# Kernel optimization log

Measured on AMD Instinct MI355X. Metric: run time of the kernel, lower is better.

Reference implementation:

```python
import jax, jax.numpy as jnp
import numpy as np

NUM_HEADS = 4

def setup_inputs() -> dict:
    key = jax.random.key(0)
    ks = jax.random.split(key, 9)
    total_nodes, d, hidden, B = 262144, 256, 256, 8192
    node_embeddings = jax.random.normal(ks[0], (total_nodes, d), dtype=jnp.float32)
    segment_ids = jnp.sort(jax.random.randint(ks[1], (total_nodes,), 0, B, dtype=jnp.int32))
    # learnable params (MultiheadAttention packed qkv, out_proj, query, output_proj)
    s = 0.05
    query = jax.random.normal(ks[2], (1, d), dtype=jnp.float32)
    in_proj_w = jax.random.normal(ks[3], (3 * d, d), dtype=jnp.float32) * s
    in_proj_b = jax.random.normal(ks[4], (3 * d,), dtype=jnp.float32) * s
    out_proj_w = jax.random.normal(ks[5], (d, d), dtype=jnp.float32) * s
    out_proj_b = jax.random.normal(ks[6], (d,), dtype=jnp.float32) * s
    output_proj_w = jax.random.normal(ks[7], (hidden, d), dtype=jnp.float32) * s
    output_proj_b = jax.random.normal(ks[8], (hidden,), dtype=jnp.float32) * s
    return {
        "node_embeddings": node_embeddings,
        "query": query,
        "in_proj_w": in_proj_w,
        "in_proj_b": in_proj_b,
        "out_proj_w": out_proj_w,
        "out_proj_b": out_proj_b,
        "output_proj_w": output_proj_w,
        "output_proj_b": output_proj_b,
        "segment_ids": segment_ids,
        "batch_size": B,
    }


def reference(node_embeddings, query, in_proj_w, in_proj_b, out_proj_w, out_proj_b,
              output_proj_w, output_proj_b, segment_ids, batch_size):
    # Ragged single-query cross-attention pooling (eval mode: dropout off).
    N, d = node_embeddings.shape
    H = NUM_HEADS
    dh = d // H
    Wq, Wk, Wv = in_proj_w[:d], in_proj_w[d:2 * d], in_proj_w[2 * d:]
    bq, bk, bv = in_proj_b[:d], in_proj_b[d:2 * d], in_proj_b[2 * d:]
    # query is shared across all graphs; torch MHA scales q by 1/sqrt(dh)
    q = ((query @ Wq.T + bq) / jnp.sqrt(jnp.asarray(dh, node_embeddings.dtype))).reshape(H, dh)
    k = (node_embeddings @ Wk.T + bk).reshape(N, H, dh)
    v = (node_embeddings @ Wv.T + bv).reshape(N, H, dh)
    scores = jnp.einsum('nhd,hd->nh', k, q)  # [N, H]
    # segment-wise stable softmax over ragged node groups
    m = jax.ops.segment_max(scores, segment_ids, num_segments=batch_size)  # [B, H]
    m = jnp.where(jnp.isfinite(m), m, 0.0)
    e = jnp.exp(scores - m[segment_ids])  # [N, H]
    denom = jax.ops.segment_sum(e, segment_ids, num_segments=batch_size)  # [B, H]
    numer = jax.ops.segment_sum(e[:, :, None] * v, segment_ids, num_segments=batch_size)  # [B, H, dh]
    attn = jnp.where(denom[:, :, None] > 0, numer / jnp.maximum(denom[:, :, None], 1e-30), 0.0)
    pooled = attn.reshape(batch_size, d) @ out_proj_w.T + out_proj_b  # MHA out_proj
    out = pooled @ output_proj_w.T + output_proj_b  # [B, hidden]
    # empty graphs -> zeros (matches torch branch), not just bias
    counts = jax.ops.segment_sum(jnp.ones((N,), out.dtype), segment_ids, num_segments=batch_size)
    return jnp.where(counts[:, None] > 0, out, 0.0)
```

## Files before the change

### kernel.cpp

```cpp
#include <hip/hip_runtime.h>
#include <hip/hip_bf16.h>
#include <stdint.h>

typedef __attribute__((ext_vector_type(8))) short short8;
typedef __attribute__((ext_vector_type(4))) float f32x4;

#define DEV static __device__ __forceinline__

DEV float half_red_bcast(float x) {
  int t;
  t = __builtin_amdgcn_update_dpp(0, __float_as_int(x), 0x111, 0xf, 0xf, true); x += __int_as_float(t);
  t = __builtin_amdgcn_update_dpp(0, __float_as_int(x), 0x112, 0xf, 0xf, true); x += __int_as_float(t);
  t = __builtin_amdgcn_update_dpp(0, __float_as_int(x), 0x114, 0xf, 0xf, true); x += __int_as_float(t);
  t = __builtin_amdgcn_update_dpp(0, __float_as_int(x), 0x118, 0xf, 0xf, true); x += __int_as_float(t);
  t = __builtin_amdgcn_update_dpp(0, __float_as_int(x), 0x142, 0xa, 0xf, true); x += __int_as_float(t);
  return __int_as_float(__builtin_amdgcn_ds_swizzle(__float_as_int(x), 0x3E0));
}

DEV void gload16(const void* g, void* lds) {
  __builtin_amdgcn_global_load_lds(
      (const __attribute__((address_space(1))) void*)g,
      (__attribute__((address_space(3))) void*)lds, 16, 0, 0);
}

__global__ __launch_bounds__(256) void k_prep(
    const float* __restrict__ query, const float* __restrict__ in_w,
    const float* __restrict__ in_b, const float* __restrict__ Wo,
    const float* __restrict__ bo, const float* __restrict__ Wu,
    const float* __restrict__ bu, const int* __restrict__ seg,
    float* __restrict__ wq_ws, float* __restrict__ ch_ws,
    float* __restrict__ btot, __hip_bfloat16* __restrict__ mtt,
    int* __restrict__ starts, int N, int B)
{
  __shared__ float sh[256];
  int t = threadIdx.x, bid = blockIdx.x;
  if (bid < 4) {
    float acc = in_b[t];
    for (int c = 0; c < 256; ++c) acc += query[c] * in_w[t * 256 + c];
    sh[t] = acc * 0.125f;
    __syncthreads();
    int h = bid;
    float a = 0.f;
    for (int j = 0; j < 64; ++j) a += sh[64 * h + j] * in_w[(256 + 64 * h + j) * 256 + t];
    wq_ws[h * 256 + t] = a;
    if (t == 0) {
      float c = 0.f;
      for (int j = 0; j < 64; ++j) c += sh[64 * h + j] * in_b[256 + 64 * h + j];
      ch_ws[h] = c;
    }
  } else if (bid < 260) {
    int u = bid - 4;
    float wc = 0.f;
    for (int o = 0; o < 256; ++o) wc += Wu[u * 256 + o] * Wo[o * 256 + t];
    sh[t] = wc;
    __syncthreads();
    #pragma unroll
    for (int h = 0; h < 4; ++h) {
      float a = 0.f;
      for (int r = 0; r < 64; ++r) a += sh[64 * h + r] * in_w[(512 + 64 * h + r) * 256 + t];
      mtt[(size_t)u * 1024 + h * 256 + t] = __float2bfloat16(a);
    }
  } else if (bid == 260) {
    const float* bv = in_b + 512;
    float wob = 0.f;
    for (int c = 0; c < 256; ++c) wob += Wo[t * 256 + c] * bv[c];
    sh[t] = bo[t] + wob;
    __syncthreads();
    float a = bu[t];
    for (int o = 0; o < 256; ++o) a += Wu[t * 256 + o] * sh[o];
    btot[t] = a;
  } else {
    int idx = (bid - 261) * 256 + t;
    if (idx < N) {
      int s = seg[idx];
      int prev = (idx == 0) ? -1 : seg[idx - 1];
      for (int x = prev + 1; x <= s; ++x) starts[x] = idx;
      if (idx == N - 1) for (int x = s + 1; x <= B; ++x) starts[x] = N;
    }
  }
}

__global__ __launch_bounds__(256, 4) void k_segattn(
    const float* __restrict__ emb, const int* __restrict__ starts,
    const float* __restrict__ wq_ws, const float* __restrict__ ch_ws,
    float* __restrict__ mask, __hip_bfloat16* __restrict__ T, int B)
{
  int lane = threadIdx.x & 63;
  int g = lane >> 5, i = lane & 31, i8 = i * 8;
  int b = blockIdx.x * 4 + (threadIdx.x >> 6);
  if (b >= B) return;
  int start = starts[b], end = starts[b + 1];
  __hip_bfloat16* Tb = T + (size_t)b * 1024;

  if (start >= end) {
    if (lane == 0) mask[b] = 0.f;
    if (lane < 32) {
      uint4 z = {0u, 0u, 0u, 0u};
      *(uint4*)(Tb + 0 * 256 + lane * 8) = z;
      *(uint4*)(Tb + 1 * 256 + lane * 8) = z;
      *(uint4*)(Tb + 2 * 256 + lane * 8) = z;
      *(uint4*)(Tb + 3 * 256 + lane * 8) = z;
    }
    return;
  }
  if (lane == 0) mask[b] = 1.f;

  float4 wa0 = *(const float4*)(wq_ws + 0 * 256 + i8), wb0 = *(const float4*)(wq_ws + 0 * 256 + i8 + 4);
  float4 wa1 = *(const float4*)(wq_ws + 1 * 256 + i8), wb1 = *(const float4*)(wq_ws + 1 * 256 + i8 + 4);
  float4 wa2 = *(const float4*)(wq_ws + 2 * 256 + i8), wb2 = *(const float4*)(wq_ws + 2 * 256 + i8 + 4);
  float4 wa3 = *(const float4*)(wq_ws + 3 * 256 + i8), wb3 = *(const float4*)(wq_ws + 3 * 256 + i8 + 4);
  float ch0 = ch_ws[0], ch1 = ch_ws[1], ch2 = ch_ws[2], ch3 = ch_ws[3];

  float m0 = -1e30f, m1 = -1e30f, m2 = -1e30f, m3 = -1e30f;
  float d0 = 0.f, d1 = 0.f, d2 = 0.f, d3 = 0.f;
  float4 Sa0 = {0,0,0,0}, Sb0 = {0,0,0,0}, Sa1 = {0,0,0,0}, Sb1 = {0,0,0,0};
  float4 Sa2 = {0,0,0,0}, Sb2 = {0,0,0,0}, Sa3 = {0,0,0,0}, Sb3 = {0,0,0,0};

  int r0 = start + g; if (r0 > end - 1) r0 = end - 1;
  const float* cp = emb + (size_t)r0 * 256 + i8;
  float4 c0 = *(const float4*)cp, c1 = *(const float4*)(cp + 4);

  for (int p = start; p < end; p += 2) {
    int rn = p + 2 + g; if (rn > end - 1) rn = end - 1;
    const float* np = emb + (size_t)rn * 256 + i8;
    float4 n0 = *(const float4*)np, n1 = *(const float4*)(np + 4);

    float p0 = c0.x*wa0.x + c0.y*wa0.y + c0.z*wa0.z + c0.w*wa0.w
             + c1.x*wb0.x + c1.y*wb0.y + c1.z*wb0.z + c1.w*wb0.w;
    float p1 = c0.x*wa1.x + c0.y*wa1.y + c0.z*wa1.z + c0.w*wa1.w
             + c1.x*wb1.x + c1.y*wb1.y + c1.z*wb1.z + c1.w*wb1.w;
    float p2 = c0.x*wa2.x + c0.y*wa2.y + c0.z*wa2.z + c0.w*wa2.w
             + c1.x*wb2.x + c1.y*wb2.y + c1.z*wb2.z + c1.w*wb2.w;
    float p3 = c0.x*wa3.x + c0.y*wa3.y + c0.z*wa3.z + c0.w*wa3.w
             + c1.x*wb3.x + c1.y*wb3.y + c1.z*wb3.z + c1.w*wb3.w;

    float s0 = half_red_bcast(p0) + ch0;
    float s1 = half_red_bcast(p1) + ch1;
    float s2 = half_red_bcast(p2) + ch2;
    float s3 = half_red_bcast(p3) + ch3;

    bool valid = (p + g) < end;
    if (!valid) { s0 = -1e30f; s1 = -1e30f; s2 = -1e30f; s3 = -1e30f; }

#define HEAD(s, m, d, SA, SB)                                               \
    { if (s > m) {                                                          \
        float rs = __expf(m - s);                                           \
        d *= rs;                                                            \
        SA.x *= rs; SA.y *= rs; SA.z *= rs; SA.w *= rs;                     \
        SB.x *= rs; SB.y *= rs; SB.z *= rs; SB.w *= rs;                     \
        m = s; }                                                            \
      float e = __expf(s - m);                                              \
      d += e;                                                               \
      SA.x += e * c0.x; SA.y += e * c0.y; SA.z += e * c0.z; SA.w += e * c0.w;\
      SB.x += e * c1.x; SB.y += e * c1.y; SB.z += e * c1.z; SB.w += e * c1.w; }
    HEAD(s0, m0, d0, Sa0, Sb0)
    HEAD(s1, m1, d1, Sa1, Sb1)
    HEAD(s2, m2, d2, Sa2, Sb2)
    HEAD(s3, m3, d3, Sa3, Sb3)
#undef HEAD
    c0 = n0; c1 = n1;
  }

#define FIN(mh, dh, SA, SB, h)                                              \
  { float om = __shfl_xor(mh, 32), od = __shfl_xor(dh, 32);                 \
    float mst = fmaxf(mh, om);                                              \
    float a0 = __expf(mh - mst), a1 = __expf(om - mst);                     \
    float sc = a0 / (dh * a0 + od * a1);                                    \
    float t0 = SA.x*sc, t1 = SA.y*sc, t2 = SA.z*sc, t3 = SA.w*sc;           \
    float t4 = SB.x*sc, t5 = SB.y*sc, t6 = SB.z*sc, t7 = SB.w*sc;           \
    t0 += __shfl_xor(t0, 32); t1 += __shfl_xor(t1, 32);                     \
    t2 += __shfl_xor(t2, 32); t3 += __shfl_xor(t3, 32);                     \
    t4 += __shfl_xor(t4, 32); t5 += __shfl_xor(t5, 32);                     \
    t6 += __shfl_xor(t6, 32); t7 += __shfl_xor(t7, 32);                     \
    if (g == 0) {                                                           \
      union { __hip_bfloat16 v[8]; uint4 u; } pk;                           \
      pk.v[0] = __float2bfloat16(t0); pk.v[1] = __float2bfloat16(t1);       \
      pk.v[2] = __float2bfloat16(t2); pk.v[3] = __float2bfloat16(t3);       \
      pk.v[4] = __float2bfloat16(t4); pk.v[5] = __float2bfloat16(t5);       \
      pk.v[6] = __float2bfloat16(t6); pk.v[7] = __float2bfloat16(t7);       \
      *(uint4*)(Tb + h * 256 + i8) = pk.u; } }
  FIN(m0, d0, Sa0, Sb0, 0)
  FIN(m1, d1, Sa1, Sb1, 1)
  FIN(m2, d2, Sa2, Sb2, 2)
  FIN(m3, d3, Sa3, Sb3, 3)
#undef FIN
}

__global__ __launch_bounds__(256) void k_out(
    const __hip_bfloat16* __restrict__ T, const __hip_bfloat16* __restrict__ mtt,
    const float* __restrict__ btot, const float* __restrict__ mask,
    float* __restrict__ out)
{
  __shared__ __align__(16) char smem[16384];
  char* As = smem;
  char* Bs = smem + 8192;
  int t = threadIdx.x;
  int l = t & 63, w = t >> 6;
  int wr = w >> 1, wc = w & 1;
  int tileM = blockIdx.y * 64, tileN = blockIdx.x * 64;

  const char* Tb = (const char*)T;
  const char* Mb = (const char*)mtt;
  int chunk = (l & 7) ^ ((l >> 3) & 7);
  f32x4 acc[2][2] = {};

  for (int kk = 0; kk < 1024; kk += 64) {
    #pragma unroll
    for (int i = 0; i < 2; ++i) {
      int row = (w * 2 + i) * 8 + (l >> 3);
      gload16(Tb + (size_t)(tileM + row) * 2048 + kk * 2 + chunk * 16,
              As + (w * 2 + i) * 1024);
      gload16(Mb + (size_t)(tileN + row) * 2048 + kk * 2 + chunk * 16,
              Bs + (w * 2 + i) * 1024);
    }
    __syncthreads();
    #pragma unroll
    for (int ks = 0; ks < 64; ks += 32) {
      short8 a[2], bf[2];
      int kbyte = (ks + (l >> 4) * 8) * 2;
      #pragma unroll
      for (int i = 0; i < 2; ++i) {
        int row = wr * 32 + i * 16 + (l & 15);
        a[i] = *(const short8*)(As + row * 128 + (kbyte ^ ((row & 7) << 4)));
        int crow = wc * 32 + i * 16 + (l & 15);
        bf[i] = *(const short8*)(Bs + crow * 128 + (kbyte ^ ((crow & 7) << 4)));
      }
      #pragma unroll
      for (int i = 0; i < 2; ++i)
        #pragma unroll
        for (int j = 0; j < 2; ++j)
          acc[i][j] = __builtin_amdgcn_mfma_f32_16x16x32_bf16(a[i], bf[j], acc[i][j], 0, 0, 0);
    }
    __syncthreads();
  }

  int cl = l & 15, rq = l >> 4;
  #pragma unroll
  for (int i = 0; i < 2; ++i)
    #pragma unroll
    for (int j = 0; j < 2; ++j) {
      int cg = tileN + wc * 32 + j * 16 + cl;
      float bt = btot[cg];
      #pragma unroll
      for (int r = 0; r < 4; ++r) {
        int rg = tileM + wr * 32 + i * 16 + rq * 4 + r;
        out[(size_t)rg * 256 + cg] = mask[rg] * (acc[i][j][r] + bt);
      }
    }
}

extern "C" void kernel_launch(void* const* d_in, const int* in_sizes, int n_in,
                              void* d_out, int out_size, void* d_ws, size_t ws_size,
                              hipStream_t stream) {
  const float* emb   = (const float*)d_in[0];
  const float* query = (const float*)d_in[1];
  const float* in_w  = (const float*)d_in[2];
  const float* in_b  = (const float*)d_in[3];
  const float* out_w = (const float*)d_in[4];
  const float* out_b = (const float*)d_in[5];
  const float* up_w  = (const float*)d_in[6];
  const float* up_b  = (const float*)d_in[7];
  const int*   seg   = (const int*)d_in[8];

  int N = in_sizes[0] / 256;
  int B = out_size / 256;

  char* wsb = (char*)d_ws;
  float* wq_ws  = (float*)(wsb + 0);
  float* ch_ws  = (float*)(wsb + 4096);
  float* btot   = (float*)(wsb + 8192);
  int*   starts = (int*)(wsb + 12288);
  float* maskp  = (float*)(wsb + 45312);
  __hip_bfloat16* mtt = (__hip_bfloat16*)(wsb + 78336);
  __hip_bfloat16* Tp  = (__hip_bfloat16*)(wsb + 602624);

  int nb_bounds = (N + 255) / 256;
  k_prep<<<dim3(261 + nb_bounds), dim3(256), 0, stream>>>(
      query, in_w, in_b, out_w, out_b, up_w, up_b, seg,
      wq_ws, ch_ws, btot, mtt, starts, N, B);
  k_segattn<<<dim3((B + 3) / 4), dim3(256), 0, stream>>>(
      emb, starts, wq_ws, ch_ws, maskp, Tp, B);
  k_out<<<dim3(4, B / 64), dim3(256), 0, stream>>>(Tp, mtt, btot, maskp, (float*)d_out);
}
```

Baseline: 90.17 us.

## Double-buffer LDS in output GEMM and split mtt prep across more blocks

The output GEMM kernel now uses two LDS buffers, issuing the global-to-LDS loads for the next K step before computing on the current one, so memory latency can overlap MFMA work. The prep kernel spreads the mtt weight-fusion computation over four times as many blocks, one per head, so that stage has more parallelism. The trade-off is doubled LDS per block, which may lower occupancy, and recomputing the Wu·Wo row product four times per row. There is also a possible hazard: the next stage's async LDS loads are issued with only one barrier per iteration and no explicit wait on the loads.

```diff
diff --git a/kernel.cpp b/kernel.cpp
--- a/kernel.cpp
+++ b/kernel.cpp
@@ -48,19 +48,16 @@
       for (int j = 0; j < 64; ++j) c += sh[64 * h + j] * in_b[256 + 64 * h + j];
       ch_ws[h] = c;
     }
-  } else if (bid < 260) {
-    int u = bid - 4;
+  } else if (bid < 1028) {
+    int u = (bid - 4) >> 2, h = (bid - 4) & 3;
     float wc = 0.f;
     for (int o = 0; o < 256; ++o) wc += Wu[u * 256 + o] * Wo[o * 256 + t];
     sh[t] = wc;
     __syncthreads();
-    #pragma unroll
-    for (int h = 0; h < 4; ++h) {
-      float a = 0.f;
-      for (int r = 0; r < 64; ++r) a += sh[64 * h + r] * in_w[(512 + 64 * h + r) * 256 + t];
-      mtt[(size_t)u * 1024 + h * 256 + t] = __float2bfloat16(a);
-    }
-  } else if (bid == 260) {
+    float a = 0.f;
+    for (int r = 0; r < 64; ++r) a += sh[64 * h + r] * in_w[(512 + 64 * h + r) * 256 + t];
+    mtt[(size_t)u * 1024 + h * 256 + t] = __float2bfloat16(a);
+  } else if (bid == 1028) {
     const float* bv = in_b + 512;
     float wob = 0.f;
     for (int c = 0; c < 256; ++c) wob += Wo[t * 256 + c] * bv[c];
@@ -70,7 +67,7 @@
     for (int o = 0; o < 256; ++o) a += Wu[t * 256 + o] * sh[o];
     btot[t] = a;
   } else {
-    int idx = (bid - 261) * 256 + t;
+    int idx = (bid - 1029) * 256 + t;
     if (idx < N) {
       int s = seg[idx];
       int prev = (idx == 0) ? -1 : seg[idx - 1];
@@ -191,9 +188,7 @@
     const float* __restrict__ btot, const float* __restrict__ mask,
     float* __restrict__ out)
 {
-  __shared__ __align__(16) char smem[16384];
-  char* As = smem;
-  char* Bs = smem + 8192;
+  __shared__ __align__(16) char smem[32768];
   int t = threadIdx.x;
   int l = t & 63, w = t >> 6;
   int wr = w >> 1, wc = w & 1;
@@ -202,18 +197,35 @@
   const char* Tb = (const char*)T;
   const char* Mb = (const char*)mtt;
   int chunk = (l & 7) ^ ((l >> 3) & 7);
+
+  const char* aSrc[2]; const char* bSrc[2]; int ldsOff[2];
+  #pragma unroll
+  for (int i = 0; i < 2; ++i) {
+    int row = (w * 2 + i) * 8 + (l >> 3);
+    aSrc[i] = Tb + (size_t)(tileM + row) * 2048 + chunk * 16;
+    bSrc[i] = Mb + (size_t)(tileN + row) * 2048 + chunk * 16;
+    ldsOff[i] = (w * 2 + i) * 1024;
+  }
+
   f32x4 acc[2][2] = {};
 
-  for (int kk = 0; kk < 1024; kk += 64) {
-    #pragma unroll
-    for (int i = 0; i < 2; ++i) {
-      int row = (w * 2 + i) * 8 + (l >> 3);
-      gload16(Tb + (size_t)(tileM + row) * 2048 + kk * 2 + chunk * 16,
-              As + (w * 2 + i) * 1024);
-      gload16(Mb + (size_t)(tileN + row) * 2048 + kk * 2 + chunk * 16,
-              Bs + (w * 2 + i) * 1024);
-    }
-    __syncthreads();
+#define STAGE(step, base)                                                   \
+  { int kb = (step) * 128;                                                  \
+    _Pragma("unroll")                                                       \
+    for (int i = 0; i < 2; ++i) {                                           \
+      gload16(aSrc[i] + kb, smem + (base) + ldsOff[i]);                     \
+      gload16(bSrc[i] + kb, smem + (base) + 8192 + ldsOff[i]);              \
+    } }
+
+  STAGE(0, 0);
+  __syncthreads();
+
+  int dbuf = 0;
+  for (int step = 0; step < 16; ++step) {
+    int base = dbuf << 14;
+    if (step + 1 < 16) STAGE(step + 1, base ^ 16384);
+    const char* As = smem + base;
+    const char* Bs = smem + base + 8192;
     #pragma unroll
     for (int ks = 0; ks < 64; ks += 32) {
       short8 a[2], bf[2];
@@ -232,7 +244,9 @@
           acc[i][j] = __builtin_amdgcn_mfma_f32_16x16x32_bf16(a[i], bf[j], acc[i][j], 0, 0, 0);
     }
     __syncthreads();
-  }
+    dbuf ^= 1;
+  }
+#undef STAGE
 
   int cl = l & 15, rq = l >> 4;
   #pragma unroll
@@ -275,7 +289,7 @@
   __hip_bfloat16* Tp  = (__hip_bfloat16*)(wsb + 602624);
 
   int nb_bounds = (N + 255) / 256;
-  k_prep<<<dim3(261 + nb_bounds), dim3(256), 0, stream>>>(
+  k_prep<<<dim3(1029 + nb_bounds), dim3(256), 0, stream>>>(
       query, in_w, in_b, out_w, out_b, up_w, up_b, seg,
       wq_ws, ch_ws, btot, mtt, starts, N, B);
   k_segattn<<<dim3((B + 3) / 4), dim3(256), 0, stream>>>(
```

Result: slower. 94.45 us (+4.7%).

## Move weight-folding blocks into attention kernel and use exp2 with prescaled scores

Applied to the files above, without the earlier changes.

The output-side weight folding (mtt and btot) moves out of the prep kernel and into extra blocks appended to the attention kernel's grid. That work now runs alongside the memory-bound segment attention instead of serializing ahead of it. The query/key fold is prescaled by log2(e), so the softmax can use exp2 directly and skip the multiply inside __expf. In exchange, the extra blocks take CU slots while attention runs, and the attention kernel gains shared memory and more arguments.

```diff
diff --git a/kernel.cpp b/kernel.cpp
--- a/kernel.cpp
+++ b/kernel.cpp
@@ -23,13 +23,12 @@
       (__attribute__((address_space(3))) void*)lds, 16, 0, 0);
 }
 
+#define LOG2E 1.44269504088896340736f
+
 __global__ __launch_bounds__(256) void k_prep(
     const float* __restrict__ query, const float* __restrict__ in_w,
-    const float* __restrict__ in_b, const float* __restrict__ Wo,
-    const float* __restrict__ bo, const float* __restrict__ Wu,
-    const float* __restrict__ bu, const int* __restrict__ seg,
+    const float* __restrict__ in_b, const int* __restrict__ seg,
     float* __restrict__ wq_ws, float* __restrict__ ch_ws,
-    float* __restrict__ btot, __hip_bfloat16* __restrict__ mtt,
     int* __restrict__ starts, int N, int B)
 {
   __shared__ float sh[256];
@@ -42,35 +41,14 @@
     int h = bid;
     float a = 0.f;
     for (int j = 0; j < 64; ++j) a += sh[64 * h + j] * in_w[(256 + 64 * h + j) * 256 + t];
-    wq_ws[h * 256 + t] = a;
+    wq_ws[h * 256 + t] = a * LOG2E;
     if (t == 0) {
       float c = 0.f;
       for (int j = 0; j < 64; ++j) c += sh[64 * h + j] * in_b[256 + 64 * h + j];
-      ch_ws[h] = c;
-    }
-  } else if (bid < 260) {
-    int u = bid - 4;
-    float wc = 0.f;
-    for (int o = 0; o < 256; ++o) wc += Wu[u * 256 + o] * Wo[o * 256 + t];
-    sh[t] = wc;
-    __syncthreads();
-    #pragma unroll
-    for (int h = 0; h < 4; ++h) {
-      float a = 0.f;
-      for (int r = 0; r < 64; ++r) a += sh[64 * h + r] * in_w[(512 + 64 * h + r) * 256 + t];
-      mtt[(size_t)u * 1024 + h * 256 + t] = __float2bfloat16(a);
-    }
-  } else if (bid == 260) {
-    const float* bv = in_b + 512;
-    float wob = 0.f;
-    for (int c = 0; c < 256; ++c) wob += Wo[t * 256 + c] * bv[c];
-    sh[t] = bo[t] + wob;
-    __syncthreads();
-    float a = bu[t];
-    for (int o = 0; o < 256; ++o) a += Wu[t * 256 + o] * sh[o];
-    btot[t] = a;
+      ch_ws[h] = c * LOG2E;
+    }
   } else {
-    int idx = (bid - 261) * 256 + t;
+    int idx = (bid - 4) * 256 + t;
     if (idx < N) {
       int s = seg[idx];
       int prev = (idx == 0) ? -1 : seg[idx - 1];
@@ -83,11 +61,45 @@
 __global__ __launch_bounds__(256, 4) void k_segattn(
     const float* __restrict__ emb, const int* __restrict__ starts,
     const float* __restrict__ wq_ws, const float* __restrict__ ch_ws,
-    float* __restrict__ mask, __hip_bfloat16* __restrict__ T, int B)
+    float* __restrict__ mask, __hip_bfloat16* __restrict__ T, int B, int nB,
+    const float* __restrict__ in_w, const float* __restrict__ in_b,
+    const float* __restrict__ Wo, const float* __restrict__ bo,
+    const float* __restrict__ Wu, const float* __restrict__ bu,
+    __hip_bfloat16* __restrict__ mtt, float* __restrict__ btot)
 {
-  int lane = threadIdx.x & 63;
+  __shared__ float sh[256];
+  int t = threadIdx.x;
+
+  if (blockIdx.x >= (unsigned)nB) {
+    int bid = blockIdx.x - nB;
+    if (bid < 256) {
+      int u = bid;
+      float wc = 0.f;
+      for (int o = 0; o < 256; ++o) wc += Wu[u * 256 + o] * Wo[o * 256 + t];
+      sh[t] = wc;
+      __syncthreads();
+      #pragma unroll
+      for (int h = 0; h < 4; ++h) {
+        float a = 0.f;
+        for (int r = 0; r < 64; ++r) a += sh[64 * h + r] * in_w[(512 + 64 * h + r) * 256 + t];
+        mtt[(size_t)u * 1024 + h * 256 + t] = __float2bfloat16(a);
+      }
+    } else {
+      const float* bv = in_b + 512;
+      float wob = 0.f;
+      for (int c = 0; c < 256; ++c) wob += Wo[t * 256 + c] * bv[c];
+      sh[t] = bo[t] + wob;
+      __syncthreads();
+      float a = bu[t];
+      for (int o = 0; o < 256; ++o) a += Wu[t * 256 + o] * sh[o];
+      btot[t] = a;
+    }
+    return;
+  }
+
+  int lane = t & 63;
   int g = lane >> 5, i = lane & 31, i8 = i * 8;
-  int b = blockIdx.x * 4 + (threadIdx.x >> 6);
+  int b = blockIdx.x * 4 + (t >> 6);
   if (b >= B) return;
   int start = starts[b], end = starts[b + 1];
   __hip_bfloat16* Tb = T + (size_t)b * 1024;
@@ -144,12 +156,12 @@
 
 #define HEAD(s, m, d, SA, SB)                                               \
     { if (s > m) {                                                          \
-        float rs = __expf(m - s);                                           \
+        float rs = __builtin_exp2f(m - s);                                  \
         d *= rs;                                                            \
         SA.x *= rs; SA.y *= rs; SA.z *= rs; SA.w *= rs;                     \
         SB.x *= rs; SB.y *= rs; SB.z *= rs; SB.w *= rs;                     \
         m = s; }                                                            \
-      float e = __expf(s - m);                                              \
+      float e = __builtin_exp2f(s - m);                                     \
       d += e;                                                               \
       SA.x += e * c0.x; SA.y += e * c0.y; SA.z += e * c0.z; SA.w += e * c0.w;\
       SB.x += e * c1.x; SB.y += e * c1.y; SB.z += e * c1.z; SB.w += e * c1.w; }
@@ -164,7 +176,7 @@
 #define FIN(mh, dh, SA, SB, h)                                              \
   { float om = __shfl_xor(mh, 32), od = __shfl_xor(dh, 32);                 \
     float mst = fmaxf(mh, om);                                              \
-    float a0 = __expf(mh - mst), a1 = __expf(om - mst);                     \
+    float a0 = __builtin_exp2f(mh - mst), a1 = __builtin_exp2f(om - mst);   \
     float sc = a0 / (dh * a0 + od * a1);                                    \
     float t0 = SA.x*sc, t1 = SA.y*sc, t2 = SA.z*sc, t3 = SA.w*sc;           \
     float t4 = SB.x*sc, t5 = SB.y*sc, t6 = SB.z*sc, t7 = SB.w*sc;           \
@@ -275,10 +287,11 @@
   __hip_bfloat16* Tp  = (__hip_bfloat16*)(wsb + 602624);
 
   int nb_bounds = (N + 255) / 256;
-  k_prep<<<dim3(261 + nb_bounds), dim3(256), 0, stream>>>(
-      query, in_w, in_b, out_w, out_b, up_w, up_b, seg,
-      wq_ws, ch_ws, btot, mtt, starts, N, B);
-  k_segattn<<<dim3((B + 3) / 4), dim3(256), 0, stream>>>(
-      emb, starts, wq_ws, ch_ws, maskp, Tp, B);
+  int nB = (B + 3) / 4;
+  k_prep<<<dim3(4 + nb_bounds), dim3(256), 0, stream>>>(
+      query, in_w, in_b, seg, wq_ws, ch_ws, starts, N, B);
+  k_segattn<<<dim3(nB + 257), dim3(256), 0, stream>>>(
+      emb, starts, wq_ws, ch_ws, maskp, Tp, B, nB,
+      in_w, in_b, out_w, out_b, up_w, up_b, mtt, btot);
   k_out<<<dim3(4, B / 64), dim3(256), 0, stream>>>(Tp, mtt, btot, maskp, (float*)d_out);
 }
```

New measurement: 89.88 us. Within noise of the previous version (-0.3%).
